# Optimization experiments

Hardware: AMD Instinct MI355X
Metric: run time of the kernel (lower is better)

The kernel has to match this reference:

```python
import jax, jax.numpy as jnp
import numpy as np

B, N, IN_C, OUT_C, HID, H = 4, 2048, 3, 1, 256, 8
V = HID // H  # v_dim per head
LOCALITIES = (50, 30, 60, 80)  # down=loc[0], PA0=loc[0], PA1=loc[1], up=loc[-1] (as in torch code)


def _gelu(x):
    return jax.nn.gelu(x, approximate=False)  # torch F.gelu default is exact erf


def _pos_att(m_dist, x, r, w, locality):
    # m_dist: [N,N], x: [B,N,HID], r: [H,1,1], w: [H,HID,V]
    scale = jnp.tan(0.25 * np.pi * (1.0 - 1e-7) * (1.0 + jnp.sin(r)))  # [H,1,1]
    sd = m_dist[None, :, :] * scale  # [H,N,N]
    if locality <= 100:
        thr = jnp.quantile(sd, locality / 100.0, axis=-1, keepdims=True)  # [H,N,1]
        sd = jnp.where(sd <= thr, sd, jnp.inf)
    att = jax.nn.softmax(-sd, axis=-1)  # masked entries -> 0
    value = jnp.einsum('bnj,hjk->bhnk', x, w)   # [B,H,N,V]
    out = jnp.einsum('hjn,bhnk->bhjk', att, value)  # [B,H,N,V]
    b, j = out.shape[0], out.shape[2]
    out = out.transpose(0, 2, 1, 3).reshape(b, j, -1)  # [B,N,HID]
    return _gelu(out)


def setup_inputs() -> dict:
    key = jax.random.key(0)
    ks = jax.random.split(key, 32)
    rn = lambda i, shape: jax.random.normal(ks[i], shape, dtype=jnp.float32)
    s = 0.02
    z = lambda d: jnp.zeros((d,), dtype=jnp.float32)
    return {
        'x': rn(0, (B, N, IN_C)),
        'm_dist0': jax.random.uniform(ks[1], (N, N), dtype=jnp.float32),
        'm_dist1': jax.random.uniform(ks[2], (N, N), dtype=jnp.float32),
        'm_dist2': jax.random.uniform(ks[3], (N, N), dtype=jnp.float32),
        'm_dist3': jax.random.uniform(ks[4], (N, N), dtype=jnp.float32),
        'en_w': rn(5, (IN_C, HID)) * s, 'en_b': z(HID),
        'down_r': rn(6, (H, 1, 1)), 'down_w': rn(7, (H, HID, V)) * s,
        'pa0_r': rn(8, (H, 1, 1)), 'pa0_w': rn(9, (H, HID, V)) * s,
        'pa1_r': rn(10, (H, 1, 1)), 'pa1_w': rn(11, (H, HID, V)) * s,
        'mlp0_w1': rn(12, (HID, HID)) * s, 'mlp0_b1': z(HID),
        'mlp0_w2': rn(13, (HID, HID)) * s, 'mlp0_b2': z(HID),
        'w0_w': rn(14, (HID, HID)) * s, 'w0_b': z(HID),
        'mlp1_w1': rn(15, (HID, HID)) * s, 'mlp1_b1': z(HID),
        'mlp1_w2': rn(16, (HID, HID)) * s, 'mlp1_b2': z(HID),
        'w1_w': rn(17, (HID, HID)) * s, 'w1_b': z(HID),
        'up_r': rn(18, (H, 1, 1)), 'up_w': rn(19, (H, HID, V)) * s,
        'de1_w': rn(20, (HID, HID)) * s, 'de1_b': z(HID),
        'de2_w': rn(21, (HID, OUT_C)) * s, 'de2_b': z(OUT_C),
    }


def reference(x, m_dist0, m_dist1, m_dist2, m_dist3, en_w, en_b,
              down_r, down_w, pa0_r, pa0_w, pa1_r, pa1_w,
              mlp0_w1, mlp0_b1, mlp0_w2, mlp0_b2, w0_w, w0_b,
              mlp1_w1, mlp1_b1, mlp1_w2, mlp1_b2, w1_w, w1_b,
              up_r, up_w, de1_w, de1_b, de2_w, de2_b):
    h = _gelu(x @ en_w + en_b)
    h = _pos_att(m_dist0, h, down_r, down_w, LOCALITIES[0])
    # block 0 (PA[0] uses localities[0], m_dists[1])
    a = _pos_att(m_dist1, h, pa0_r, pa0_w, LOCALITIES[0])
    h = _gelu((_gelu(a @ mlp0_w1 + mlp0_b1) @ mlp0_w2 + mlp0_b2) + (h @ w0_w + w0_b))
    # block 1 (PA[1] uses localities[1], m_dists[2])
    a = _pos_att(m_dist2, h, pa1_r, pa1_w, LOCALITIES[1])
    h = _gelu((_gelu(a @ mlp1_w1 + mlp1_b1) @ mlp1_w2 + mlp1_b2) + (h @ w1_w + w1_b))
    h = _pos_att(m_dist3, h, up_r, up_w, LOCALITIES[3])
    h = _gelu(h @ de1_w + de1_b)
    return h @ de2_w + de2_b
```

## Files before the change

### kernel.cpp

```cpp
#include <hip/hip_runtime.h>

#define NB 4
#define NN 2048
#define HIDDEN 256
#define NH 8
#define VD 32

typedef float f4 __attribute__((ext_vector_type(4)));

__device__ __forceinline__ float gelu_f(float v) {
    return 0.5f * v * (1.0f + erff(v * 0.7071067811865475f));
}

__global__ void k_encode(const float* __restrict__ x, const float* __restrict__ w,
                         const float* __restrict__ b, float* __restrict__ out) {
    int id = blockIdx.x * 256 + threadIdx.x;
    int c = id & 255, rn = id >> 8;
    float acc = b[c];
    acc += x[rn * 3 + 0] * w[c] + x[rn * 3 + 1] * w[256 + c] + x[rn * 3 + 2] * w[512 + c];
    out[id] = gelu_f(acc);
}

__global__ __launch_bounds__(256) void k_thrsel4(
        const float* __restrict__ m0, const float* __restrict__ m1,
        const float* __restrict__ m2, const float* __restrict__ m3,
        const float* __restrict__ r0, const float* __restrict__ r1,
        const float* __restrict__ r2, const float* __restrict__ r3,
        int k0, int k1, int k2, int k3,
        float* __restrict__ thr, float* __restrict__ mmin, float* __restrict__ invD)
{
    __shared__ float rowf[NN];
    __shared__ unsigned hist[256];
    __shared__ float redf[32];
    __shared__ unsigned redu[4];
    __shared__ unsigned s_bin, s_below;
    const int row = blockIdx.x, t = threadIdx.x;
    const int c = blockIdx.y;
    const int lane = t & 63, wid = t >> 6;
    const float* mb = (c == 0) ? m0 : (c == 1) ? m1 : (c == 2) ? m2 : m3;
    const float* rv = (c == 0) ? r0 : (c == 1) ? r1 : (c == 2) ? r2 : r3;
    const int kcount = (c == 0) ? k0 : (c == 1) ? k1 : (c == 2) ? k2 : k3;
    const float* mr = mb + (size_t)row * NN;

    float lmin = 3.4e38f;
    for (int i = t; i < NN; i += 256) { float v = mr[i]; rowf[i] = v; lmin = fminf(lmin, v); }
#pragma unroll
    for (int d = 32; d > 0; d >>= 1) lmin = fminf(lmin, __shfl_xor(lmin, d, 64));
    if (lane == 0) redf[wid] = lmin;
    __syncthreads();
    const float rmin = fminf(fminf(redf[0], redf[1]), fminf(redf[2], redf[3]));

    unsigned prefix = 0; int want = kcount;
    const unsigned hmasks[4] = {0u, 0xFF000000u, 0xFFFF0000u, 0xFFFFFF00u};
    for (int pass = 0; pass < 4; ++pass) {
        const int shift = 24 - 8 * pass;
        hist[t] = 0;
        __syncthreads();
        const unsigned hm = hmasks[pass];
        for (int i = t; i < NN; i += 256) {
            unsigned u = __float_as_uint(rowf[i]);
            u ^= (u & 0x80000000u) ? 0xFFFFFFFFu : 0x80000000u;
            if ((u & hm) == (prefix & hm))
                atomicAdd(&hist[(u >> shift) & 255u], 1u);
        }
        __syncthreads();
        const unsigned cnt = hist[t];
        unsigned v = cnt;
#pragma unroll
        for (int d = 1; d < 64; d <<= 1) {
            unsigned o = __shfl_up(v, d, 64);
            if (lane >= d) v += o;
        }
        if (lane == 63) redu[wid] = v;
        __syncthreads();
        unsigned woff = 0;
#pragma unroll
        for (int w = 0; w < 3; w++) if (w < wid) woff += redu[w];
        const unsigned incl = v + woff;
        const unsigned below = incl - cnt;
        if (incl >= (unsigned)want && below < (unsigned)want) { s_bin = (unsigned)t; s_below = below; }
        __syncthreads();
        want -= (int)s_below;
        prefix |= (s_bin << shift);
    }
    unsigned ku = prefix;
    ku = (ku & 0x80000000u) ? (ku & 0x7FFFFFFFu) : ~ku;
    const float tf = __uint_as_float(ku);

    const float cc = (float)(0.25 * 3.141592653589793 * (1.0 - 1e-7));
    float sch[NH], lacc[NH];
#pragma unroll
    for (int h = 0; h < NH; h++) { sch[h] = tanf(cc * (1.0f + sinf(rv[h]))); lacc[h] = 0.f; }
    for (int i = t; i < NN; i += 256) {
        float v = rowf[i];
        if (v <= tf) {
            float d = v - rmin;
#pragma unroll
            for (int h = 0; h < NH; h++) lacc[h] += expf(-sch[h] * d);
        }
    }
#pragma unroll
    for (int h = 0; h < NH; h++) {
#pragma unroll
        for (int d = 32; d > 0; d >>= 1) lacc[h] += __shfl_xor(lacc[h], d, 64);
    }
    if (lane == 0) {
#pragma unroll
        for (int h = 0; h < NH; h++) redf[wid * 8 + h] = lacc[h];
    }
    __syncthreads();
    if (t < NH)
        invD[(c * NH + t) * NN + row] = 1.0f / (redf[t] + redf[8 + t] + redf[16 + t] + redf[24 + t]);
    if (t == 0) { thr[c * NN + row] = tf; mmin[c * NN + row] = rmin; }
}

__global__ __launch_bounds__(256) void k_gemm(const float* __restrict__ A,
        const float* __restrict__ Wm, const float* __restrict__ bias,
        const float* __restrict__ addsrc, float* __restrict__ Cm, int act, int wmode)
{
    __shared__ float AsT[64 * 68];
    __shared__ float Ws[64 * 68];
    const int r0 = blockIdx.x * 64;
    const int c0 = blockIdx.y * 64;
    const int t = threadIdx.x;
    const int ty = t >> 4, tx = t & 15;
    float acc[4][4] = {};
    for (int k0 = 0; k0 < 256; k0 += 64) {
        __syncthreads();
#pragma unroll
        for (int l = 0; l < 16; l++) {
            int lin = l * 256 + t;
            int rr = lin >> 6, kk = lin & 63;
            AsT[kk * 68 + rr] = A[(size_t)(r0 + rr) * 256 + k0 + kk];
            Ws[rr * 68 + kk] = wmode
                ? Wm[(size_t)((c0 + kk) >> 5) * (HIDDEN * VD) + (size_t)(k0 + rr) * VD + ((c0 + kk) & 31)]
                : Wm[(size_t)(k0 + rr) * 256 + c0 + kk];
        }
        __syncthreads();
#pragma unroll 8
        for (int kk = 0; kk < 64; kk++) {
            const float4 a4 = *(const float4*)&AsT[kk * 68 + ty * 4];
            const float4 w4 = *(const float4*)&Ws[kk * 68 + tx * 4];
            float av[4] = {a4.x, a4.y, a4.z, a4.w};
            float wv[4] = {w4.x, w4.y, w4.z, w4.w};
#pragma unroll
            for (int q = 0; q < 4; q++)
#pragma unroll
                for (int p = 0; p < 4; p++)
                    acc[q][p] = fmaf(av[q], wv[p], acc[q][p]);
        }
    }
#pragma unroll
    for (int q = 0; q < 4; q++) {
        int r = r0 + ty * 4 + q;
#pragma unroll
        for (int p = 0; p < 4; p++) {
            int c = c0 + tx * 4 + p;
            float v = acc[q][p];
            if (bias) v += bias[c];
            if (addsrc) v += addsrc[(size_t)r * 256 + c];
            if (act) v = gelu_f(v);
            Cm[(size_t)r * 256 + c] = v;
        }
    }
}

template<int WMODE>
__global__ __launch_bounds__(256) void k_gemm9(const float* __restrict__ A,
        const float* __restrict__ Wm, float* __restrict__ G0, float* __restrict__ G1)
{
    __shared__ float AsT[64 * 68];
    __shared__ float Ws[64 * 68];
    const int r0 = blockIdx.x * 64;
    const int c0 = blockIdx.y * 64;
    const int kbase = blockIdx.z * 128;
    float* __restrict__ G = blockIdx.z ? G1 : G0;
    const int t = threadIdx.x;
    const int ty = t >> 4, tx = t & 15;
    float acc[4][4] = {};
    for (int kh = 0; kh < 128; kh += 64) {
        const int k0 = kbase + kh;
        __syncthreads();
#pragma unroll
        for (int l = 0; l < 16; l++) {
            int lin = l * 256 + t;
            int rr = lin >> 6, kk = lin & 63;
            AsT[kk * 68 + rr] = A[(size_t)(r0 + rr) * 256 + k0 + kk];
            Ws[rr * 68 + kk] = WMODE
                ? Wm[(size_t)((c0 + kk) >> 5) * (HIDDEN * VD) + (size_t)(k0 + rr) * VD + ((c0 + kk) & 31)]
                : Wm[(size_t)(k0 + rr) * 256 + c0 + kk];
        }
        __syncthreads();
#pragma unroll 8
        for (int kk = 0; kk < 64; kk++) {
            const float4 a4 = *(const float4*)&AsT[kk * 68 + ty * 4];
            const float4 w4 = *(const float4*)&Ws[kk * 68 + tx * 4];
            float av[4] = {a4.x, a4.y, a4.z, a4.w};
            float wv[4] = {w4.x, w4.y, w4.z, w4.w};
#pragma unroll
            for (int q = 0; q < 4; q++)
#pragma unroll
                for (int p = 0; p < 4; p++)
                    acc[q][p] = fmaf(av[q], wv[p], acc[q][p]);
        }
    }
#pragma unroll
    for (int q = 0; q < 4; q++) {
        const int r = r0 + ty * 4 + q;
        f4 st;
#pragma unroll
        for (int p = 0; p < 4; p++) st[p] = acc[q][p];
        *(f4*)&G[(size_t)r * 256 + c0 + tx * 4] = st;
    }
}

__global__ __launch_bounds__(256) void k_gemmcomb(const float* __restrict__ g0,
        const float* __restrict__ g1, const float* __restrict__ bias,
        const float* __restrict__ addsrc, float* __restrict__ out, int act)
{
    int gid = blockIdx.x * 256 + threadIdx.x;
    int idx = gid * 4;
    int c = idx & 255;
    f4 a = *(const f4*)&g0[idx];
    f4 b = *(const f4*)&g1[idx];
    f4 s;
#pragma unroll
    for (int k = 0; k < 4; k++) s[k] = a[k] + b[k];
    if (bias) {
        f4 bb = *(const f4*)&bias[c];
#pragma unroll
        for (int k = 0; k < 4; k++) s[k] += bb[k];
    }
    if (addsrc) {
        f4 r = *(const f4*)&addsrc[idx];
#pragma unroll
        for (int k = 0; k < 4; k++) s[k] += r[k];
    }
    if (act) {
#pragma unroll
        for (int k = 0; k < 4; k++) s[k] = gelu_f(s[k]);
    }
    *(f4*)&out[idx] = s;
}

#define TJA 32
__global__ __launch_bounds__(256, 2) void k_attapply8(
    const float* __restrict__ m, const float* __restrict__ v2,
    const float* __restrict__ rv, const float* __restrict__ thr,
    const float* __restrict__ mmin,
    float* __restrict__ P0, float* __restrict__ P1,
    float* __restrict__ P2, float* __restrict__ P3, int jlen)
{
    __shared__ float EsA[128 * 36];
    __shared__ float VsA[TJA * 132];
    __shared__ float EsB[128 * 36];
    __shared__ float VsB[TJA * 132];
    const int head = blockIdx.x >> 4;
    const int i0 = (blockIdx.x & 15) * 128;
    const int jbase = blockIdx.y * jlen;
    const int by = blockIdx.y;
    float* __restrict__ P = (by == 0) ? P0 : (by == 1) ? P1 : (by == 2) ? P2 : P3;
    const int t = threadIdx.x;
    const int tx = t & 15, ty = t >> 4;
    const int txm = t & 7, tym = t >> 3;
    const int c4 = t & 31, jw = t >> 5;
    const int bbv = c4 >> 3, kkv = (c4 & 7) * 4;
    const float cc = (float)(0.25 * 3.141592653589793 * (1.0 - 1e-7));
    const float scale = tanf(cc * (1.0f + sinf(rv[head])));

    float thr_r[4], mmn_r[4];
#pragma unroll
    for (int q = 0; q < 4; q++) {
        thr_r[q] = thr[i0 + q * 32 + tym];
        mmn_r[q] = mmin[i0 + q * 32 + tym];
    }

    float acc[8][8];
#pragma unroll
    for (int q = 0; q < 8; q++)
#pragma unroll
        for (int p = 0; p < 8; p++) acc[q][p] = 0.f;

    f4 pm[4], pv[4];
    const int NT = jlen / TJA;

#define A_LOAD(S)                                                              \
    do {                                                                       \
        const int j0 = jbase + (S) * TJA;                                      \
        _Pragma("unroll")                                                      \
        for (int q = 0; q < 4; q++)                                            \
            pm[q] = *(const f4*)&m[(size_t)(i0 + q * 32 + tym) * NN + j0 + 4 * txm]; \
        _Pragma("unroll")                                                      \
        for (int l = 0; l < 4; l++)                                            \
            pv[l] = *(const f4*)&v2[(((size_t)bbv * NN) + j0 + l * 8 + jw) * HIDDEN + head * VD + kkv]; \
    } while (0)

#define A_STORE(ES, VS)                                                        \
    do {                                                                       \
        _Pragma("unroll")                                                      \
        for (int q = 0; q < 4; q++) {                                          \
            f4 ev;                                                             \
            _Pragma("unroll")                                                  \
            for (int d = 0; d < 4; d++) {                                      \
                float e = 0.f;                                                 \
                if (pm[q][d] <= thr_r[q]) e = expf(-scale * (pm[q][d] - mmn_r[q])); \
                ev[d] = e;                                                     \
            }                                                                  \
            *(f4*)&ES[(q * 32 + tym) * 36 + 4 * txm] = ev;                     \
        }                                                                      \
        _Pragma("unroll")                                                      \
        for (int l = 0; l < 4; l++)                                            \
            *(f4*)&VS[(l * 8 + jw) * 132 + 4 * c4] = pv[l];                    \
    } while (0)

#define A_COMPUTE(ES, VS)                                                      \
    do {                                                                       \
        for (int jc = 0; jc < TJA; jc += 4) {                                  \
            f4 ev[8], va[4], vb[4];                                            \
            _Pragma("unroll")                                                  \
            for (int q = 0; q < 8; q++)                                        \
                ev[q] = *(const f4*)&ES[(q * 16 + ty) * 36 + jc];              \
            _Pragma("unroll")                                                  \
            for (int d = 0; d < 4; d++) {                                      \
                va[d] = *(const f4*)&VS[(jc + d) * 132 + 4 * tx];              \
                vb[d] = *(const f4*)&VS[(jc + d) * 132 + 64 + 4 * tx];         \
            }                                                                  \
            _Pragma("unroll")                                                  \
            for (int d = 0; d < 4; d++) {                                      \
                _Pragma("unroll")                                              \
                for (int q = 0; q < 8; q++) {                                  \
                    const float e = ev[q][d];                                  \
                    _Pragma("unroll")                                          \
                    for (int p = 0; p < 4; p++) {                              \
                        acc[q][p]     = fmaf(e, va[d][p], acc[q][p]);          \
                        acc[q][p + 4] = fmaf(e, vb[d][p], acc[q][p + 4]);      \
                    }                                                          \
                }                                                              \
            }                                                                  \
        }                                                                      \
    } while (0)

    A_LOAD(0);
    A_STORE(EsA, VsA);
    __syncthreads();

    for (int s = 0; s < NT; s += 2) {
        if (s + 1 < NT) A_LOAD(s + 1);
        A_COMPUTE(EsA, VsA);
        if (s + 1 < NT) {
            A_STORE(EsB, VsB);
            __syncthreads();
        }
        if (s + 2 < NT) A_LOAD(s + 2);
        if (s + 1 < NT) A_COMPUTE(EsB, VsB);
        if (s + 2 < NT) {
            A_STORE(EsA, VsA);
            __syncthreads();
        }
    }
#undef A_LOAD
#undef A_STORE
#undef A_COMPUTE

    const int bba = tx >> 3, kka = (tx & 7) * 4;
#pragma unroll
    for (int q = 0; q < 8; q++) {
        const int gi = i0 + q * 16 + ty;
        f4 sa, sb;
#pragma unroll
        for (int p = 0; p < 4; p++) { sa[p] = acc[q][p]; sb[p] = acc[q][p + 4]; }
        *(f4*)&P[(((size_t)bba * NN) + gi) * HIDDEN + head * VD + kka] = sa;
        *(f4*)&P[(((size_t)(bba + 2) * NN) + gi) * HIDDEN + head * VD + kka] = sb;
    }
}

__global__ __launch_bounds__(256) void k_attcombine(const float* __restrict__ p1,
        const float* __restrict__ p2, const float* __restrict__ p3,
        const float* __restrict__ invD, float* __restrict__ io)
{
    int gid = blockIdx.x * 256 + threadIdx.x;
    int idx = gid * 4;
    int hid = idx & (HIDDEN - 1);
    int i = (idx >> 8) & (NN - 1);
    float sD = invD[(hid >> 5) * NN + i];
    f4 a = *(const f4*)&io[idx];
    f4 b = *(const f4*)&p1[idx];
    f4 s;
#pragma unroll
    for (int k = 0; k < 4; k++) s[k] = a[k] + b[k];
    if (p2) {
        f4 c = *(const f4*)&p2[idx];
        f4 d = *(const f4*)&p3[idx];
#pragma unroll
        for (int k = 0; k < 4; k++) s[k] += c[k] + d[k];
    }
#pragma unroll
    for (int k = 0; k < 4; k++) s[k] = gelu_f(s[k] * sD);
    *(f4*)&io[idx] = s;
}

__global__ void k_decode(const float* __restrict__ a, const float* __restrict__ w,
                         const float* __restrict__ b, float* __restrict__ out) {
    int gid = blockIdx.x * 256 + threadIdx.x;
    int row = gid >> 6, lane = threadIdx.x & 63;
    const float* ar = a + (size_t)row * HIDDEN;
    float s = ar[lane] * w[lane] + ar[lane + 64] * w[lane + 64]
            + ar[lane + 128] * w[lane + 128] + ar[lane + 192] * w[lane + 192];
    for (int off = 32; off > 0; off >>= 1) s += __shfl_down(s, off);
    if (lane == 0) out[row] = s + b[0];
}

extern "C" void kernel_launch(void* const* d_in, const int* in_sizes, int n_in,
                              void* d_out, int out_size, void* d_ws, size_t ws_size,
                              hipStream_t stream)
{
    (void)in_sizes; (void)n_in; (void)out_size;
    const float* x      = (const float*)d_in[0];
    const float* m0     = (const float*)d_in[1];
    const float* m1     = (const float*)d_in[2];
    const float* m2     = (const float*)d_in[3];
    const float* m3     = (const float*)d_in[4];
    const float* en_w   = (const float*)d_in[5];
    const float* en_b   = (const float*)d_in[6];
    const float* down_r = (const float*)d_in[7];
    const float* down_w = (const float*)d_in[8];
    const float* pa0_r  = (const float*)d_in[9];
    const float* pa0_w  = (const float*)d_in[10];
    const float* pa1_r  = (const float*)d_in[11];
    const float* pa1_w  = (const float*)d_in[12];
    const float* mlp0_w1= (const float*)d_in[13];
    const float* mlp0_b1= (const float*)d_in[14];
    const float* mlp0_w2= (const float*)d_in[15];
    const float* mlp0_b2= (const float*)d_in[16];
    const float* w0_w   = (const float*)d_in[17];
    const float* w0_b   = (const float*)d_in[18];
    const float* mlp1_w1= (const float*)d_in[19];
    const float* mlp1_b1= (const float*)d_in[20];
    const float* mlp1_w2= (const float*)d_in[21];
    const float* mlp1_b2= (const float*)d_in[22];
    const float* w1_w   = (const float*)d_in[23];
    const float* w1_b   = (const float*)d_in[24];
    const float* up_r   = (const float*)d_in[25];
    const float* up_w   = (const float*)d_in[26];
    const float* de1_w  = (const float*)d_in[27];
    const float* de1_b  = (const float*)d_in[28];
    const float* de2_w  = (const float*)d_in[29];
    const float* de2_b  = (const float*)d_in[30];
    float* out = (float*)d_out;

    float* WS = (float*)d_ws;
    const size_t SZ = (size_t)NB * NN * HIDDEN;
    float* Hb   = WS;
    float* Ab   = Hb + SZ;
    float* Vb   = Ab + SZ;
    float* T1   = Vb + SZ;
    float* THR4 = T1 + SZ;
    float* MMIN4= THR4 + 4 * NN;
    float* INVD4= MMIN4 + 4 * NN;
    float* P2   = INVD4 + 4 * NH * NN;
    float* P3   = P2 + SZ;
    const size_t need4 = (size_t)((P3 + SZ) - WS) * sizeof(float);
    const int JS = (ws_size >= need4) ? 4 : 2;
    float* T3   = Vb;

    auto gemm = [&](const float* A, const float* W, const float* bias,
                    const float* add, float* dst, int act, int wmode) {
        if (JS >= 4) {
            if (wmode)
                hipLaunchKernelGGL((k_gemm9<1>), dim3(128, 4, 2), dim3(256), 0, stream,
                                   A, W, P2, P3);
            else
                hipLaunchKernelGGL((k_gemm9<0>), dim3(128, 4, 2), dim3(256), 0, stream,
                                   A, W, P2, P3);
            hipLaunchKernelGGL(k_gemmcomb, dim3((int)(SZ / 4 / 256)), dim3(256), 0, stream,
                               P2, P3, bias, add, dst, act);
        } else {
            hipLaunchKernelGGL(k_gemm, dim3(128, 4), dim3(256), 0, stream,
                               A, W, bias, add, dst, act, wmode);
        }
    };

    hipLaunchKernelGGL(k_thrsel4, dim3(NN, 4), dim3(256), 0, stream,
                       m0, m1, m2, m3, down_r, pa0_r, pa1_r, up_r,
                       1024, 1024, 615, 1638, THR4, MMIN4, INVD4);

    auto posatt = [&](int c, const float* src, float* dst2, const float* md,
                      const float* r, const float* w) {
        gemm(src, w, nullptr, nullptr, Vb, 0, 1);
        hipLaunchKernelGGL(k_attapply8, dim3(128, JS), dim3(256), 0, stream,
                           md, Vb, r, THR4 + c * NN, MMIN4 + c * NN,
                           dst2, T1, P2, P3, NN / JS);
        hipLaunchKernelGGL(k_attcombine, dim3((int)(SZ / 4 / 256)), dim3(256), 0, stream,
                           T1, (JS >= 4) ? P2 : (const float*)nullptr,
                           (JS >= 4) ? P3 : (const float*)nullptr,
                           INVD4 + c * NH * NN, dst2);
    };

    float* curH = Hb; float* oth = Ab;
    hipLaunchKernelGGL(k_encode, dim3(8192), dim3(256), 0, stream, x, en_w, en_b, curH);

    posatt(0, curH, oth, m0, down_r, down_w);
    { float* tmp = curH; curH = oth; oth = tmp; }

    posatt(1, curH, oth, m1, pa0_r, pa0_w);
    gemm(curH, w0_w, w0_b, nullptr, T3, 0, 0);
    gemm(oth, mlp0_w1, mlp0_b1, nullptr, T1, 1, 0);
    gemm(T1, mlp0_w2, mlp0_b2, T3, oth, 1, 0);
    { float* tmp = curH; curH = oth; oth = tmp; }

    posatt(2, curH, oth, m2, pa1_r, pa1_w);
    gemm(curH, w1_w, w1_b, nullptr, T3, 0, 0);
    gemm(oth, mlp1_w1, mlp1_b1, nullptr, T1, 1, 0);
    gemm(T1, mlp1_w2, mlp1_b2, T3, oth, 1, 0);
    { float* tmp = curH; curH = oth; oth = tmp; }

    posatt(3, curH, oth, m3, up_r, up_w);
    { float* tmp = curH; curH = oth; oth = tmp; }

    gemm(curH, de1_w, de1_b, nullptr, T1, 1, 0);
    hipLaunchKernelGGL(k_decode, dim3(2048), dim3(256), 0, stream, T1, de2_w, de2_b, out);
}
```

Baseline: 844.6 us.

## Use 128x128 register-tiled GEMM with 4-way split-K and prefetch

Replaces the 64x64 split-K-by-2 GEMM with a 128x128 tile kernel using an 8x8 per-thread register tile, a K split of 4 across blockIdx.z, and register prefetch of the next K-slab while computing the current one. The combine kernel now sums four partial buffers. This raises arithmetic intensity per shared-memory load and aims to hide global load latency. In exchange it needs two extra full-size workspace buffers and more combine traffic, and the larger workspace requirement may push the code onto the JS=2 fallback path if the workspace is too small.

```diff
diff --git a/kernel.cpp b/kernel.cpp
--- a/kernel.cpp
+++ b/kernel.cpp
@@ -165,57 +165,113 @@
     }
 }
 
+#define GKX 32
 template<int WMODE>
-__global__ __launch_bounds__(256) void k_gemm9(const float* __restrict__ A,
-        const float* __restrict__ Wm, float* __restrict__ G0, float* __restrict__ G1)
-{
-    __shared__ float AsT[64 * 68];
-    __shared__ float Ws[64 * 68];
-    const int r0 = blockIdx.x * 64;
-    const int c0 = blockIdx.y * 64;
-    const int kbase = blockIdx.z * 128;
-    float* __restrict__ G = blockIdx.z ? G1 : G0;
+__global__ __launch_bounds__(256, 2) void k_gemm10(const float* __restrict__ A,
+        const float* __restrict__ Wm,
+        float* __restrict__ G0, float* __restrict__ G1,
+        float* __restrict__ G2, float* __restrict__ G3)
+{
+    __shared__ float As[128 * 36];
+    __shared__ float Ws[GKX * 132];
+    const int r0 = blockIdx.x * 128;
+    const int c0 = blockIdx.y * 128;
+    const int kbase = blockIdx.z * 64;
+    const int bz = blockIdx.z;
+    float* __restrict__ G = (bz == 0) ? G0 : (bz == 1) ? G1 : (bz == 2) ? G2 : G3;
     const int t = threadIdx.x;
-    const int ty = t >> 4, tx = t & 15;
-    float acc[4][4] = {};
-    for (int kh = 0; kh < 128; kh += 64) {
-        const int k0 = kbase + kh;
-        __syncthreads();
-#pragma unroll
-        for (int l = 0; l < 16; l++) {
-            int lin = l * 256 + t;
-            int rr = lin >> 6, kk = lin & 63;
-            AsT[kk * 68 + rr] = A[(size_t)(r0 + rr) * 256 + k0 + kk];
-            Ws[rr * 68 + kk] = WMODE
-                ? Wm[(size_t)((c0 + kk) >> 5) * (HIDDEN * VD) + (size_t)(k0 + rr) * VD + ((c0 + kk) & 31)]
-                : Wm[(size_t)(k0 + rr) * 256 + c0 + kk];
-        }
-        __syncthreads();
-#pragma unroll 8
-        for (int kk = 0; kk < 64; kk++) {
-            const float4 a4 = *(const float4*)&AsT[kk * 68 + ty * 4];
-            const float4 w4 = *(const float4*)&Ws[kk * 68 + tx * 4];
-            float av[4] = {a4.x, a4.y, a4.z, a4.w};
-            float wv[4] = {w4.x, w4.y, w4.z, w4.w};
-#pragma unroll
-            for (int q = 0; q < 4; q++)
-#pragma unroll
-                for (int p = 0; p < 4; p++)
-                    acc[q][p] = fmaf(av[q], wv[p], acc[q][p]);
-        }
-    }
-#pragma unroll
-    for (int q = 0; q < 4; q++) {
-        const int r = r0 + ty * 4 + q;
-        f4 st;
-#pragma unroll
-        for (int p = 0; p < 4; p++) st[p] = acc[q][p];
-        *(f4*)&G[(size_t)r * 256 + c0 + tx * 4] = st;
-    }
-}
-
-__global__ __launch_bounds__(256) void k_gemmcomb(const float* __restrict__ g0,
-        const float* __restrict__ g1, const float* __restrict__ bias,
+    const int tx = t & 15, ty = t >> 4;
+    const int txm = t & 7, tym = t >> 3;
+    const int c4 = t & 31, jw = t >> 5;
+
+    float acc[8][8];
+#pragma unroll
+    for (int q = 0; q < 8; q++)
+#pragma unroll
+        for (int p = 0; p < 8; p++) acc[q][p] = 0.f;
+
+    f4 pm[4], pv[4];
+    const int NT = 64 / GKX;
+
+#define G_LOAD(S)                                                              \
+    do {                                                                       \
+        const int k0 = kbase + (S) * GKX;                                      \
+        _Pragma("unroll")                                                      \
+        for (int q = 0; q < 4; q++)                                            \
+            pm[q] = *(const f4*)&A[(size_t)(r0 + q * 32 + tym) * 256 + k0 + 4 * txm]; \
+        _Pragma("unroll")                                                      \
+        for (int l = 0; l < 4; l++) {                                          \
+            const int kk = k0 + l * 8 + jw;                                    \
+            const int c = c0 + 4 * c4;                                         \
+            if (WMODE)                                                         \
+                pv[l] = *(const f4*)&Wm[(size_t)(c >> 5) * (HIDDEN * VD) + (size_t)kk * VD + (c & 31)]; \
+            else                                                               \
+                pv[l] = *(const f4*)&Wm[(size_t)kk * 256 + c];                 \
+        }                                                                      \
+    } while (0)
+
+#define G_STORE()                                                              \
+    do {                                                                       \
+        _Pragma("unroll")                                                      \
+        for (int q = 0; q < 4; q++)                                            \
+            *(f4*)&As[(q * 32 + tym) * 36 + 4 * txm] = pm[q];                  \
+        _Pragma("unroll")                                                      \
+        for (int l = 0; l < 4; l++)                                            \
+            *(f4*)&Ws[(l * 8 + jw) * 132 + 4 * c4] = pv[l];                    \
+    } while (0)
+
+    G_LOAD(0);
+    G_STORE();
+    __syncthreads();
+
+    for (int s = 0; s < NT; s++) {
+        if (s + 1 < NT) G_LOAD(s + 1);
+        for (int jc = 0; jc < GKX; jc += 4) {
+            f4 ev[8], va[4], vb[4];
+#pragma unroll
+            for (int q = 0; q < 8; q++)
+                ev[q] = *(const f4*)&As[(q * 16 + ty) * 36 + jc];
+#pragma unroll
+            for (int d = 0; d < 4; d++) {
+                va[d] = *(const f4*)&Ws[(jc + d) * 132 + 4 * tx];
+                vb[d] = *(const f4*)&Ws[(jc + d) * 132 + 64 + 4 * tx];
+            }
+#pragma unroll
+            for (int d = 0; d < 4; d++) {
+#pragma unroll
+                for (int q = 0; q < 8; q++) {
+                    const float e = ev[q][d];
+#pragma unroll
+                    for (int p = 0; p < 4; p++) {
+                        acc[q][p]     = fmaf(e, va[d][p], acc[q][p]);
+                        acc[q][p + 4] = fmaf(e, vb[d][p], acc[q][p + 4]);
+                    }
+                }
+            }
+        }
+        if (s + 1 < NT) {
+            __syncthreads();
+            G_STORE();
+            __syncthreads();
+        }
+    }
+#undef G_LOAD
+#undef G_STORE
+
+#pragma unroll
+    for (int q = 0; q < 8; q++) {
+        const int r = r0 + q * 16 + ty;
+        f4 sa, sb;
+#pragma unroll
+        for (int p = 0; p < 4; p++) { sa[p] = acc[q][p]; sb[p] = acc[q][p + 4]; }
+        *(f4*)&G[(size_t)r * 256 + c0 + 4 * tx] = sa;
+        *(f4*)&G[(size_t)r * 256 + c0 + 64 + 4 * tx] = sb;
+    }
+}
+
+__global__ __launch_bounds__(256) void k_gemmcomb4(const float* __restrict__ g0,
+        const float* __restrict__ g1, const float* __restrict__ g2,
+        const float* __restrict__ g3, const float* __restrict__ bias,
         const float* __restrict__ addsrc, float* __restrict__ out, int act)
 {
     int gid = blockIdx.x * 256 + threadIdx.x;
@@ -223,9 +279,11 @@
     int c = idx & 255;
     f4 a = *(const f4*)&g0[idx];
     f4 b = *(const f4*)&g1[idx];
+    f4 e = *(const f4*)&g2[idx];
+    f4 f = *(const f4*)&g3[idx];
     f4 s;
 #pragma unroll
-    for (int k = 0; k < 4; k++) s[k] = a[k] + b[k];
+    for (int k = 0; k < 4; k++) s[k] = (a[k] + b[k]) + (e[k] + f[k]);
     if (bias) {
         f4 bb = *(const f4*)&bias[c];
 #pragma unroll
@@ -459,21 +517,23 @@
     float* INVD4= MMIN4 + 4 * NN;
     float* P2   = INVD4 + 4 * NH * NN;
     float* P3   = P2 + SZ;
-    const size_t need4 = (size_t)((P3 + SZ) - WS) * sizeof(float);
-    const int JS = (ws_size >= need4) ? 4 : 2;
+    float* P4   = P3 + SZ;
+    float* P5   = P4 + SZ;
+    const size_t needG = (size_t)((P5 + SZ) - WS) * sizeof(float);
+    const int JS = (ws_size >= needG) ? 4 : 2;
     float* T3   = Vb;
 
     auto gemm = [&](const float* A, const float* W, const float* bias,
                     const float* add, float* dst, int act, int wmode) {
         if (JS >= 4) {
             if (wmode)
-                hipLaunchKernelGGL((k_gemm9<1>), dim3(128, 4, 2), dim3(256), 0, stream,
-                                   A, W, P2, P3);
+                hipLaunchKernelGGL((k_gemm10<1>), dim3(64, 2, 4), dim3(256), 0, stream,
+                                   A, W, P2, P3, P4, P5);
             else
-                hipLaunchKernelGGL((k_gemm9<0>), dim3(128, 4, 2), dim3(256), 0, stream,
-                                   A, W, P2, P3);
-            hipLaunchKernelGGL(k_gemmcomb, dim3((int)(SZ / 4 / 256)), dim3(256), 0, stream,
-                               P2, P3, bias, add, dst, act);
+                hipLaunchKernelGGL((k_gemm10<0>), dim3(64, 2, 4), dim3(256), 0, stream,
+                                   A, W, P2, P3, P4, P5);
+            hipLaunchKernelGGL(k_gemmcomb4, dim3((int)(SZ / 4 / 256)), dim3(256), 0, stream,
+                               P2, P3, P4, P5, bias, add, dst, act);
         } else {
             hipLaunchKernelGGL(k_gemm, dim3(128, 4), dim3(256), 0, stream,
                                A, W, bias, add, dst, act, wmode);
```

Result: slower. 865.5 us (+2.5%).
